# Performance work log

Measured on AMD Instinct MI355X. Metric: run time of the kernel, lower is better.

## Reference

```python
import jax, jax.numpy as jnp
import numpy as np

B, S, D = 32, 4096, 64          # batch, max seq len, input_dim
P, STRIDE, H = 8, 4, 512        # patch_size, patch_stride, hidden_size
T = (S - P) // STRIDE + 1       # static max token count (sample 0 has length S)
EPS = 1e-6


def setup_inputs() -> dict:
    key = jax.random.key(0)
    k1, k2, k3 = jax.random.split(key, 3)
    x = jax.random.normal(k1, (B, S, D), dtype=jnp.float32)
    lengths = jax.random.randint(k2, (B,), P, S + 1)
    lengths = lengths.at[0].set(S)  # at least one full-length sample -> max_tokens == T
    W = jax.random.normal(k3, (P * D, H), dtype=jnp.float32) / np.sqrt(P * D)
    b = jnp.zeros((H,), dtype=jnp.float32)
    scale = jnp.ones((H,), dtype=jnp.float32)  # RMSNorm scale
    return {"x": x, "lengths": lengths, "W": W, "b": b, "scale": scale}


def _patch(x, lengths):
    # number of tokens per sample: len(range(0, max(L-P+1, 1), STRIDE))
    n_tok = jnp.where(lengths >= P, (lengths - P) // STRIDE + 1, 1)  # [B]
    # gather positions for every (token, within-patch) slot
    pos = jnp.arange(T)[:, None] * STRIDE + jnp.arange(P)[None, :]   # [T, P]
    tokens = x[:, pos, :]                                            # [B, T, P, D]
    valid = (pos[None, :, :] < lengths[:, None, None]) \
          & (jnp.arange(T)[None, :, None] < n_tok[:, None, None])    # [B, T, P]
    tokens = jnp.where(valid[..., None], tokens, 0.0)
    return tokens.reshape(B, T, P * D), n_tok


def reference(x, lengths, W, b, scale):
    tokens, token_lengths = _patch(x, lengths)        # [B, T, P*D], [B]
    h = tokens @ W + b                                # proj -> [B, T, H]
    rms = jnp.sqrt(jnp.mean(h * h, axis=-1, keepdims=True) + EPS)
    hidden = h / rms * scale                          # RMSNorm
    return hidden, token_lengths, tokens
```

## Files before the change

kernel.cpp:

```cpp
#include <hip/hip_runtime.h>
#include <hip/hip_bf16.h>

constexpr int Bc = 32, Sc = 4096, Dc = 64, Pc = 8, STRIDEc = 4, Hc = 512;
constexpr int Tc = (Sc - Pc) / STRIDEc + 1;
constexpr int Kc = Pc * Dc;
constexpr float EPSc = 1e-6f;
constexpr int PITCH = 40;

typedef __bf16 bf16x8 __attribute__((ext_vector_type(8)));
typedef unsigned short ushort8 __attribute__((ext_vector_type(8)));
typedef float f32x4 __attribute__((ext_vector_type(4)));

__device__ __forceinline__ int n_tok_of(int len) {
    return (len >= Pc) ? ((len - Pc) / STRIDEc + 1) : 1;
}

__device__ __forceinline__ unsigned short f2bf(float f) {
    unsigned u = __builtin_bit_cast(unsigned, f);
    u = (u + 0x7FFFu + ((u >> 16) & 1u)) >> 16;
    return (unsigned short)u;
}

__global__ __launch_bounds__(256) void prep_kernel(
        const float* __restrict__ W, const int* __restrict__ lengths,
        unsigned short* __restrict__ Wt, float* __restrict__ out_tl) {
    __shared__ float tile[32][33];
    const int k0 = blockIdx.x * 32, n0 = blockIdx.y * 32;
    const int r = threadIdx.x >> 3, c = (threadIdx.x & 7) * 4;
    const float4 v = *(const float4*)(W + (size_t)(k0 + r) * Hc + n0 + c);
    tile[c + 0][r] = v.x;
    tile[c + 1][r] = v.y;
    tile[c + 2][r] = v.z;
    tile[c + 3][r] = v.w;
    __syncthreads();
    ushort4 o;
    o.x = f2bf(tile[r][c + 0]);
    o.y = f2bf(tile[r][c + 1]);
    o.z = f2bf(tile[r][c + 2]);
    o.w = f2bf(tile[r][c + 3]);
    *(ushort4*)(Wt + (size_t)blockIdx.x * (Hc * 32) + (size_t)(n0 + r) * 32 + c) = o;
    if (blockIdx.x == 0 && blockIdx.y == 0 && threadIdx.x < Bc)
        out_tl[threadIdx.x] = (float)n_tok_of(lengths[threadIdx.x]);
}

__global__ __launch_bounds__(256, 2) void fused_kernel(
        const float* __restrict__ x, const int* __restrict__ lengths,
        const unsigned short* __restrict__ Wt, const float* __restrict__ bias,
        const float* __restrict__ scale, float* __restrict__ hidden,
        float* __restrict__ tokens) {
    const int b  = blockIdx.y;
    const int t0 = blockIdx.x * 64;
    const int len = lengths[b];
    const int ntok = n_tok_of(len);

    __shared__ unsigned short As[64 * PITCH];
    __shared__ unsigned short Bs[512 * PITCH];
    __shared__ float ssbuf[4][64];

    const int tid  = threadIdx.x;
    const int w    = tid >> 6;
    const int lane = tid & 63;
    const int l15  = lane & 15;
    const int quad = lane >> 4;

    f32x4 acc[4][8];
#pragma unroll
    for (int tt = 0; tt < 4; ++tt)
#pragma unroll
        for (int ct = 0; ct < 8; ++ct) acc[tt][ct] = (f32x4){0.f, 0.f, 0.f, 0.f};

    const float* xb   = x + (size_t)b * (Sc * Dc);
    float*       tokb = tokens + (size_t)b * Tc * Kc;

    int   a_r[2], a_c[2];  bool a_tv[2];  const float* a_src[2];
#pragma unroll
    for (int it = 0; it < 2; ++it) {
        const int l = tid + it * 256;
        a_r[it] = l >> 3;
        a_c[it] = (l & 7) * 4;
        const int t = t0 + a_r[it];
        a_tv[it] = (t < Tc);
        a_src[it] = xb + (size_t)t * (STRIDEc * Dc);
    }

    float4  ra[2];
    ushort8 rb[8];

#pragma unroll
    for (int it = 0; it < 2; ++it) {
        const int t = t0 + a_r[it];
        const int kk = a_c[it];
        const int pos = t * STRIDEc + (kk >> 6);
        ra[it] = make_float4(0.f, 0.f, 0.f, 0.f);
        if (a_tv[it] && t < ntok && pos < len) ra[it] = *(const float4*)(a_src[it] + kk);
    }
#pragma unroll
    for (int it = 0; it < 8; ++it)
        rb[it] = *(const ushort8*)(Wt + (size_t)(tid + it * 256) * 8);

    for (int step = 0; step < 16; ++step) {
        const int k0 = step * 32;
        if (step) __syncthreads();

#pragma unroll
        for (int it = 0; it < 2; ++it) {
            const float4 v = ra[it];
            if (a_tv[it])
                *(float4*)(tokb + (size_t)(t0 + a_r[it]) * Kc + k0 + a_c[it]) = v;
            ushort4 h4;
            h4.x = f2bf(v.x); h4.y = f2bf(v.y); h4.z = f2bf(v.z); h4.w = f2bf(v.w);
            *(ushort4*)(As + a_r[it] * PITCH + a_c[it]) = h4;
        }
#pragma unroll
        for (int it = 0; it < 8; ++it) {
            const int cc = tid + it * 256;
            *(ushort8*)(Bs + (cc >> 2) * PITCH + (cc & 3) * 8) = rb[it];
        }
        __syncthreads();

        if (step < 15) {
            const int kn = k0 + 32;
#pragma unroll
            for (int it = 0; it < 2; ++it) {
                const int t = t0 + a_r[it];
                const int kk = kn + a_c[it];
                const int pos = t * STRIDEc + (kk >> 6);
                ra[it] = make_float4(0.f, 0.f, 0.f, 0.f);
                if (a_tv[it] && t < ntok && pos < len)
                    ra[it] = *(const float4*)(a_src[it] + kk);
            }
            const unsigned short* wsrc = Wt + (size_t)(step + 1) * (Hc * 32);
#pragma unroll
            for (int it = 0; it < 8; ++it)
                rb[it] = *(const ushort8*)(wsrc + (size_t)(tid + it * 256) * 8);
        }

        bf16x8 btok[4];
#pragma unroll
        for (int tt = 0; tt < 4; ++tt)
            btok[tt] = __builtin_bit_cast(bf16x8,
                *(const ushort8*)(As + (tt * 16 + l15) * PITCH + quad * 8));
#pragma unroll
        for (int ct = 0; ct < 8; ++ct) {
            bf16x8 aW = __builtin_bit_cast(bf16x8,
                *(const ushort8*)(Bs + (w * 128 + ct * 16 + l15) * PITCH + quad * 8));
#pragma unroll
            for (int tt = 0; tt < 4; ++tt)
                acc[tt][ct] = __builtin_amdgcn_mfma_f32_16x16x32_bf16(
                    aW, btok[tt], acc[tt][ct], 0, 0, 0);
        }
    }

    float ss[4] = {0.f, 0.f, 0.f, 0.f};
#pragma unroll
    for (int ct = 0; ct < 8; ++ct) {
        const f32x4 b4 = *(const f32x4*)(bias + w * 128 + ct * 16 + quad * 4);
#pragma unroll
        for (int tt = 0; tt < 4; ++tt) {
            f32x4 h = acc[tt][ct] + b4;
            acc[tt][ct] = h;
            ss[tt] += h[0] * h[0] + h[1] * h[1] + h[2] * h[2] + h[3] * h[3];
        }
    }
#pragma unroll
    for (int tt = 0; tt < 4; ++tt) {
        float s = ss[tt];
        s += __shfl_xor(s, 16);
        s += __shfl_xor(s, 32);
        if (quad == 0) ssbuf[w][tt * 16 + l15] = s;
    }
    __syncthreads();
    float rstd[4];
#pragma unroll
    for (int tt = 0; tt < 4; ++tt) {
        const int r = tt * 16 + l15;
        const float tot = ssbuf[0][r] + ssbuf[1][r] + ssbuf[2][r] + ssbuf[3][r];
        rstd[tt] = rsqrtf(tot * (1.0f / (float)Hc) + EPSc);
    }
#pragma unroll
    for (int ct = 0; ct < 8; ++ct) {
        const f32x4 s4 = *(const f32x4*)(scale + w * 128 + ct * 16 + quad * 4);
#pragma unroll
        for (int tt = 0; tt < 4; ++tt) {
            const int t = t0 + tt * 16 + l15;
            if (t < Tc) {
                f32x4 o = acc[tt][ct] * rstd[tt] * s4;
                *(f32x4*)(hidden + ((size_t)b * Tc + t) * Hc
                          + w * 128 + ct * 16 + quad * 4) = o;
            }
        }
    }
}

extern "C" void kernel_launch(void* const* d_in, const int* in_sizes, int n_in,
                              void* d_out, int out_size, void* d_ws, size_t ws_size,
                              hipStream_t stream) {
    const float* x       = (const float*)d_in[0];
    const int*   lengths = (const int*)d_in[1];
    const float* W       = (const float*)d_in[2];
    const float* bias    = (const float*)d_in[3];
    const float* scale   = (const float*)d_in[4];

    const size_t BTH = (size_t)Bc * Tc * Hc;
    float* out    = (float*)d_out;
    float* hidden = out;
    float* tl     = out + BTH;
    float* tokens = out + BTH + Bc;

    unsigned short* Wt = (unsigned short*)d_ws;

    {
        dim3 grid(Hc / 32, Hc / 32);
        prep_kernel<<<grid, 256, 0, stream>>>(W, lengths, Wt, tl);
    }
    {
        dim3 grid(16, Bc);
        fused_kernel<<<grid, 256, 0, stream>>>(x, lengths, Wt, bias, scale,
                                               hidden, tokens);
    }
}
```

Measured before the change: 180.9 us.

## Skip GEMM for padded tiles, load W fragments directly to registers, double-buffer A

Blocks whose whole token tile lies past the sample's token count skip the GEMM. They write the constant RMSNorm of the bias into hidden and zeros into tokens. For the other blocks, W bf16 fragments are loaded from global memory straight into registers in ping-pong sets instead of being staged through shared memory. The A tile is double-buffered, which cuts one barrier per step, and the outputs use nontemporal stores. The register-resident W raises register pressure, and each wave re-reads W from L2 instead of sharing it through LDS.

```diff
diff --git a/kernel.cpp b/kernel.cpp
--- a/kernel.cpp
+++ b/kernel.cpp
@@ -52,12 +52,41 @@
     const int t0 = blockIdx.x * 64;
     const int len = lengths[b];
     const int ntok = n_tok_of(len);
-
-    __shared__ unsigned short As[64 * PITCH];
-    __shared__ unsigned short Bs[512 * PITCH];
+    const int tid = threadIdx.x;
+
+    float* tokb = tokens + (size_t)b * Tc * Kc;
+
+    if (t0 >= ntok) {
+        __shared__ float red[4];
+        const int w = tid >> 6, lane = tid & 63;
+        const float2 b2 = *(const float2*)(bias + tid * 2);
+        float s = b2.x * b2.x + b2.y * b2.y;
+#pragma unroll
+        for (int off = 32; off; off >>= 1) s += __shfl_xor(s, off);
+        if (lane == 0) red[w] = s;
+        __syncthreads();
+        const float rstd = rsqrtf((red[0] + red[1] + red[2] + red[3])
+                                  * (1.0f / (float)Hc) + EPSc);
+        const int c4 = (tid & 127) * 4;
+        const f32x4 cvec = *(const f32x4*)(bias + c4) * rstd
+                         * *(const f32x4*)(scale + c4);
+        const f32x4 z = {0.f, 0.f, 0.f, 0.f};
+        float* hidb = hidden + ((size_t)b * Tc + t0) * Hc;
+        float* tokp = tokb + (size_t)t0 * Kc;
+        const int r0 = tid >> 7;
+#pragma unroll 8
+        for (int rr = r0; rr < 64; rr += 2) {
+            if (t0 + rr < Tc) {
+                __builtin_nontemporal_store(cvec, (f32x4*)(hidb + (size_t)rr * Hc + c4));
+                __builtin_nontemporal_store(z,    (f32x4*)(tokp + (size_t)rr * Kc + c4));
+            }
+        }
+        return;
+    }
+
+    __shared__ unsigned short As[2][64 * PITCH];
     __shared__ float ssbuf[4][64];
 
-    const int tid  = threadIdx.x;
     const int w    = tid >> 6;
     const int lane = tid & 63;
     const int l15  = lane & 15;
@@ -69,10 +98,9 @@
 #pragma unroll
         for (int ct = 0; ct < 8; ++ct) acc[tt][ct] = (f32x4){0.f, 0.f, 0.f, 0.f};
 
-    const float* xb   = x + (size_t)b * (Sc * Dc);
-    float*       tokb = tokens + (size_t)b * Tc * Kc;
-
-    int   a_r[2], a_c[2];  bool a_tv[2];  const float* a_src[2];
+    const float* xb = x + (size_t)b * (Sc * Dc);
+
+    int a_r[2], a_c[2];  bool a_tv[2], a_lv[2];  const float* a_src[2];
 #pragma unroll
     for (int it = 0; it < 2; ++it) {
         const int l = tid + it * 256;
@@ -80,75 +108,69 @@
         a_c[it] = (l & 7) * 4;
         const int t = t0 + a_r[it];
         a_tv[it] = (t < Tc);
+        a_lv[it] = (t < ntok);
         a_src[it] = xb + (size_t)t * (STRIDEc * Dc);
     }
 
-    float4  ra[2];
-    ushort8 rb[8];
+    f32x4   ra[2];
+    ushort8 rbA[8], rbB[8];
+
+    const unsigned short* wfrag = Wt + ((w * 128 + l15) * 32 + quad * 8);
 
 #pragma unroll
     for (int it = 0; it < 2; ++it) {
-        const int t = t0 + a_r[it];
-        const int kk = a_c[it];
-        const int pos = t * STRIDEc + (kk >> 6);
-        ra[it] = make_float4(0.f, 0.f, 0.f, 0.f);
-        if (a_tv[it] && t < ntok && pos < len) ra[it] = *(const float4*)(a_src[it] + kk);
-    }
-#pragma unroll
-    for (int it = 0; it < 8; ++it)
-        rb[it] = *(const ushort8*)(Wt + (size_t)(tid + it * 256) * 8);
-
-    for (int step = 0; step < 16; ++step) {
+        ra[it] = (f32x4){0.f, 0.f, 0.f, 0.f};
+        if (a_lv[it]) ra[it] = *(const f32x4*)(a_src[it] + a_c[it]);
+    }
+#pragma unroll
+    for (int ct = 0; ct < 8; ++ct)
+        rbA[ct] = *(const ushort8*)(wfrag + ct * 512);
+
+    auto do_step = [&](const int step, ushort8 (&rbC)[8], ushort8 (&rbN)[8]) {
+        const int p  = step & 1;
         const int k0 = step * 32;
-        if (step) __syncthreads();
-
 #pragma unroll
         for (int it = 0; it < 2; ++it) {
-            const float4 v = ra[it];
+            const f32x4 v = ra[it];
             if (a_tv[it])
-                *(float4*)(tokb + (size_t)(t0 + a_r[it]) * Kc + k0 + a_c[it]) = v;
+                __builtin_nontemporal_store(v,
+                    (f32x4*)(tokb + (size_t)(t0 + a_r[it]) * Kc + k0 + a_c[it]));
             ushort4 h4;
-            h4.x = f2bf(v.x); h4.y = f2bf(v.y); h4.z = f2bf(v.z); h4.w = f2bf(v.w);
-            *(ushort4*)(As + a_r[it] * PITCH + a_c[it]) = h4;
-        }
-#pragma unroll
-        for (int it = 0; it < 8; ++it) {
-            const int cc = tid + it * 256;
-            *(ushort8*)(Bs + (cc >> 2) * PITCH + (cc & 3) * 8) = rb[it];
+            h4.x = f2bf(v[0]); h4.y = f2bf(v[1]); h4.z = f2bf(v[2]); h4.w = f2bf(v[3]);
+            *(ushort4*)(&As[p][0] + a_r[it] * PITCH + a_c[it]) = h4;
         }
         __syncthreads();
-
+        bf16x8 btok[4];
+#pragma unroll
+        for (int tt = 0; tt < 4; ++tt)
+            btok[tt] = __builtin_bit_cast(bf16x8,
+                *(const ushort8*)(&As[p][0] + (tt * 16 + l15) * PITCH + quad * 8));
         if (step < 15) {
             const int kn = k0 + 32;
 #pragma unroll
             for (int it = 0; it < 2; ++it) {
-                const int t = t0 + a_r[it];
-                const int kk = kn + a_c[it];
-                const int pos = t * STRIDEc + (kk >> 6);
-                ra[it] = make_float4(0.f, 0.f, 0.f, 0.f);
-                if (a_tv[it] && t < ntok && pos < len)
-                    ra[it] = *(const float4*)(a_src[it] + kk);
+                ra[it] = (f32x4){0.f, 0.f, 0.f, 0.f};
+                if (a_lv[it]) ra[it] = *(const f32x4*)(a_src[it] + kn + a_c[it]);
             }
-            const unsigned short* wsrc = Wt + (size_t)(step + 1) * (Hc * 32);
-#pragma unroll
-            for (int it = 0; it < 8; ++it)
-                rb[it] = *(const ushort8*)(wsrc + (size_t)(tid + it * 256) * 8);
-        }
-
-        bf16x8 btok[4];
-#pragma unroll
-        for (int tt = 0; tt < 4; ++tt)
-            btok[tt] = __builtin_bit_cast(bf16x8,
-                *(const ushort8*)(As + (tt * 16 + l15) * PITCH + quad * 8));
+            const unsigned short* wn = wfrag + (size_t)(step + 1) * (Hc * 32);
+#pragma unroll
+            for (int ct = 0; ct < 8; ++ct)
+                rbN[ct] = *(const ushort8*)(wn + ct * 512);
+        }
 #pragma unroll
         for (int ct = 0; ct < 8; ++ct) {
-            bf16x8 aW = __builtin_bit_cast(bf16x8,
-                *(const ushort8*)(Bs + (w * 128 + ct * 16 + l15) * PITCH + quad * 8));
+            const bf16x8 aW = __builtin_bit_cast(bf16x8, rbC[ct]);
 #pragma unroll
             for (int tt = 0; tt < 4; ++tt)
                 acc[tt][ct] = __builtin_amdgcn_mfma_f32_16x16x32_bf16(
                     aW, btok[tt], acc[tt][ct], 0, 0, 0);
         }
+    };
+
+#pragma unroll
+    for (int sp = 0; sp < 8; ++sp) {
+        do_step(2 * sp,     rbA, rbB);
+        do_step(2 * sp + 1, rbB, rbA);
     }
 
     float ss[4] = {0.f, 0.f, 0.f, 0.f};
@@ -185,8 +207,9 @@
             const int t = t0 + tt * 16 + l15;
             if (t < Tc) {
                 f32x4 o = acc[tt][ct] * rstd[tt] * s4;
-                *(f32x4*)(hidden + ((size_t)b * Tc + t) * Hc
-                          + w * 128 + ct * 16 + quad * 4) = o;
+                __builtin_nontemporal_store(o,
+                    (f32x4*)(hidden + ((size_t)b * Tc + t) * Hc
+                             + w * 128 + ct * 16 + quad * 4));
             }
         }
     }
```

Result: slower. 192.6 us (+6.5%).

## Skip GEMM for fully padded token tiles and balance tile order across batches

Applied to the files above, without the earlier changes.

Blocks whose first token index is beyond the sample's token count now skip the GEMM. They compute the constant RMSNorm of the bias vector once and write it, along with zero tokens, using nontemporal stores. The tile index is reversed for half of the batches to spread heavy and light blocks across CUs. The per-element position check is dropped, since t < ntok already implies every position in the patch lies inside the length. This relies on the reference producing bias-only hidden rows for padded tokens.

```diff
diff --git a/kernel.cpp b/kernel.cpp
--- a/kernel.cpp
+++ b/kernel.cpp
@@ -49,15 +49,45 @@
         const float* __restrict__ scale, float* __restrict__ hidden,
         float* __restrict__ tokens) {
     const int b  = blockIdx.y;
-    const int t0 = blockIdx.x * 64;
+    const int t0 = ((b & 16) ? (15 - (int)blockIdx.x) : (int)blockIdx.x) * 64;
     const int len = lengths[b];
     const int ntok = n_tok_of(len);
+    const int tid = threadIdx.x;
+
+    float* tokb = tokens + (size_t)b * Tc * Kc;
+
+    if (t0 >= ntok) {
+        __shared__ float red[4];
+        const int w = tid >> 6, lane = tid & 63;
+        const float2 b2 = *(const float2*)(bias + tid * 2);
+        float s = b2.x * b2.x + b2.y * b2.y;
+#pragma unroll
+        for (int off = 32; off; off >>= 1) s += __shfl_xor(s, off);
+        if (lane == 0) red[w] = s;
+        __syncthreads();
+        const float rstd0 = rsqrtf((red[0] + red[1] + red[2] + red[3])
+                                   * (1.0f / (float)Hc) + EPSc);
+        const int c4 = (tid & 127) * 4;
+        const f32x4 cvec = *(const f32x4*)(bias + c4) * rstd0
+                         * *(const f32x4*)(scale + c4);
+        const f32x4 z = {0.f, 0.f, 0.f, 0.f};
+        float* hidb = hidden + ((size_t)b * Tc + t0) * Hc;
+        float* tokp = tokb + (size_t)t0 * Kc;
+        const int r0 = tid >> 7;
+#pragma unroll 8
+        for (int rr = r0; rr < 64; rr += 2) {
+            if (t0 + rr < Tc) {
+                __builtin_nontemporal_store(cvec, (f32x4*)(hidb + (size_t)rr * Hc + c4));
+                __builtin_nontemporal_store(z,    (f32x4*)(tokp + (size_t)rr * Kc + c4));
+            }
+        }
+        return;
+    }
 
     __shared__ unsigned short As[64 * PITCH];
     __shared__ unsigned short Bs[512 * PITCH];
     __shared__ float ssbuf[4][64];
 
-    const int tid  = threadIdx.x;
     const int w    = tid >> 6;
     const int lane = tid & 63;
     const int l15  = lane & 15;
@@ -69,10 +99,9 @@
 #pragma unroll
         for (int ct = 0; ct < 8; ++ct) acc[tt][ct] = (f32x4){0.f, 0.f, 0.f, 0.f};
 
-    const float* xb   = x + (size_t)b * (Sc * Dc);
-    float*       tokb = tokens + (size_t)b * Tc * Kc;
-
-    int   a_r[2], a_c[2];  bool a_tv[2];  const float* a_src[2];
+    const float* xb = x + (size_t)b * (Sc * Dc);
+
+    int   a_r[2], a_c[2];  bool a_tv[2], a_lv[2];  const float* a_src[2];
 #pragma unroll
     for (int it = 0; it < 2; ++it) {
         const int l = tid + it * 256;
@@ -80,6 +109,7 @@
         a_c[it] = (l & 7) * 4;
         const int t = t0 + a_r[it];
         a_tv[it] = (t < Tc);
+        a_lv[it] = (t < ntok);
         a_src[it] = xb + (size_t)t * (STRIDEc * Dc);
     }
 
@@ -88,11 +118,8 @@
 
 #pragma unroll
     for (int it = 0; it < 2; ++it) {
-        const int t = t0 + a_r[it];
-        const int kk = a_c[it];
-        const int pos = t * STRIDEc + (kk >> 6);
         ra[it] = make_float4(0.f, 0.f, 0.f, 0.f);
-        if (a_tv[it] && t < ntok && pos < len) ra[it] = *(const float4*)(a_src[it] + kk);
+        if (a_lv[it]) ra[it] = *(const float4*)(a_src[it] + a_c[it]);
     }
 #pragma unroll
     for (int it = 0; it < 8; ++it)
@@ -122,12 +149,8 @@
             const int kn = k0 + 32;
 #pragma unroll
             for (int it = 0; it < 2; ++it) {
-                const int t = t0 + a_r[it];
-                const int kk = kn + a_c[it];
-                const int pos = t * STRIDEc + (kk >> 6);
                 ra[it] = make_float4(0.f, 0.f, 0.f, 0.f);
-                if (a_tv[it] && t < ntok && pos < len)
-                    ra[it] = *(const float4*)(a_src[it] + kk);
+                if (a_lv[it]) ra[it] = *(const float4*)(a_src[it] + kn + a_c[it]);
             }
             const unsigned short* wsrc = Wt + (size_t)(step + 1) * (Hc * 32);
 #pragma unroll
```

After: 187.1 us (median of 2 runs). 1.03x slower.
